# Optimization experiments

Hardware: AMD Instinct MI355X
Metric: run time of the kernel (lower is better)

The kernel has to match this reference:

```python
import jax, jax.numpy as jnp
import numpy as np

B, N, C, H = 2, 128, 256, 8
D = C // H
SCALE = D ** -0.5
LN_EPS = 1e-5


def _layernorm(x, g, b):
    mu = jnp.mean(x, axis=-1, keepdims=True)
    var = jnp.mean((x - mu) ** 2, axis=-1, keepdims=True)
    return (x - mu) * jax.lax.rsqrt(var + LN_EPS) * g + b


def setup_inputs() -> dict:
    key = jax.random.key(0)
    ks = jax.random.split(key, 12)
    s = 0.02
    return {
        "e": jax.random.normal(ks[0], (B, N, N, C), jnp.float32),
        "mask": jnp.zeros((B, N, N, H), jnp.float32),
        "ln_g": jnp.ones((C,), jnp.float32),
        "ln_b": jnp.zeros((C,), jnp.float32),
        "W_qkv_in": jax.random.normal(ks[1], (C, 3 * C), jnp.float32) * s,
        "b_qkv_in": jnp.zeros((3 * C,), jnp.float32),
        "W_E_in": jax.random.normal(ks[2], (C, H), jnp.float32) * s,
        "b_E_in": jnp.zeros((H,), jnp.float32),
        "W_qkv_out": jax.random.normal(ks[3], (C, 3 * C), jnp.float32) * s,
        "b_qkv_out": jnp.zeros((3 * C,), jnp.float32),
        "W_E_out": jax.random.normal(ks[4], (C, H), jnp.float32) * s,
        "b_E_out": jnp.zeros((H,), jnp.float32),
        "W_O": jax.random.normal(ks[5], (2 * C, C), jnp.float32) * s,
        "b_O": jnp.zeros((C,), jnp.float32),
    }


def reference(e, mask, ln_g, ln_b, W_qkv_in, b_qkv_in, W_E_in, b_E_in,
              W_qkv_out, b_qkv_out, W_E_out, b_E_out, W_O, b_O):
    b_, n, _, c = e.shape
    e_ln = _layernorm(e, ln_g, ln_b)

    def qkv(W, bias):
        z = e_ln @ W + bias  # [B,N,N,3C]
        q, k, v = jnp.split(z, 3, axis=-1)
        rs = lambda t: t.reshape(b_, n, n, D, H)
        return rs(q) * SCALE, rs(k), rs(v)

    # --- in pass ---
    Q, K, V = qkv(W_qkv_in, b_qkv_in)
    E_in = (e_ln @ W_E_in + b_E_in)[:, :, None, :, :]       # [B,N,1,N,H]
    H_in = jnp.einsum('bijdh,bjkdh->bijkh', Q, K) + E_in
    A_in = jax.nn.softmax(H_in + mask[:, :, None, :, :], axis=3)
    Va_in = jnp.einsum('bijkh,bjkdh->bijdh', A_in, V)

    # --- out pass ---
    Q, K, V = qkv(W_qkv_out, b_qkv_out)
    E_out = (e_ln @ W_E_out + b_E_out)[:, :, :, None, :]    # [B,N,N,1,H]
    H_out = jnp.einsum('bijdh,bkjdh->bkijh', Q, K) + E_out
    A_out = jax.nn.softmax(H_out + mask[:, :, :, None, :], axis=1)
    Va_out = jnp.einsum('bkijh,bkjdh->bijdh', A_out, V)

    Va = jnp.concatenate([Va_in, Va_out], axis=-1).reshape(b_, n, n, 2 * c)
    return Va @ W_O + b_O
```

## Files before the change

kernel.cpp:

```cpp
#include <hip/hip_runtime.h>

typedef unsigned short u16;
typedef __attribute__((ext_vector_type(8))) short bf16x8;
typedef __attribute__((ext_vector_type(4))) float f32x4;

#define SCALE 0.17677669529663687f

__device__ __forceinline__ float us2f(u16 u){ return __uint_as_float(((unsigned int)u)<<16); }
__device__ __forceinline__ u16 f2us(float f){
  unsigned int x = __float_as_uint(f);
  x += 0x7fffu + ((x>>16)&1u);
  return (u16)(x>>16);
}
__device__ __forceinline__ void gl_lds16(const u16* g, u16* l){
  __builtin_amdgcn_global_load_lds(
    (const __attribute__((address_space(1))) unsigned int*)g,
    (__attribute__((address_space(3))) unsigned int*)l, 16, 0, 0);
}

__global__ __launch_bounds__(256) void ln_kernel(const float* __restrict__ e, const float* __restrict__ g,
                                                 const float* __restrict__ bb, u16* __restrict__ eln){
  int t = threadIdx.x;
  int tok = blockIdx.x*4 + (t>>6);
  int lane = t & 63;
  int c0 = lane*4;
  float4 x = *(const float4*)(e + tok*256 + c0);
  float sum = x.x+x.y+x.z+x.w;
  float sq  = x.x*x.x + x.y*x.y + x.z*x.z + x.w*x.w;
  #pragma unroll
  for (int off=32; off>=1; off>>=1){ sum += __shfl_xor(sum, off); sq += __shfl_xor(sq, off); }
  float mu = sum * 0.00390625f;
  float var = sq * 0.00390625f - mu*mu;
  float rstd = rsqrtf(var + 1e-5f);
  float4 gv = *(const float4*)(g + c0);
  float4 bv = *(const float4*)(bb + c0);
  ushort4 o;
  o.x = f2us((x.x-mu)*rstd*gv.x + bv.x);
  o.y = f2us((x.y-mu)*rstd*gv.y + bv.y);
  o.z = f2us((x.z-mu)*rstd*gv.z + bv.z);
  o.w = f2us((x.w-mu)*rstd*gv.w + bv.w);
  *(ushort4*)(eln + tok*256 + c0) = o;
}

__global__ __launch_bounds__(256) void prep_all(const float* __restrict__ Wi, const float* __restrict__ WEi,
                                                const float* __restrict__ Wo, const float* __restrict__ WEo,
                                                const float* __restrict__ WO,
                                                u16* __restrict__ WtI, u16* __restrict__ WtO,
                                                u16* __restrict__ WOt){
  int idx = blockIdx.x*256 + threadIdx.x;
  if (idx < 425984){
    int which = idx >= 212992;
    int id2 = which ? idx - 212992 : idx;
    const float* W  = which ? Wo  : Wi;
    const float* WE = which ? WEo : WEi;
    u16* Wt = which ? WtO : WtI;
    int n = id2 >> 8, k = id2 & 255;
    float v;
    if (n < 768){
      int sec = n >> 8, r = n & 255, h = r >> 5, d = r & 31;
      v = W[k*768 + sec*256 + d*8 + h];
    } else if (n < 776) v = WE[k*8 + (n-768)];
    else v = 0.f;
    Wt[id2] = f2us(v);
  } else if (idx < 557056){
    int id2 = idx - 425984;
    int n = id2 >> 9, kp = id2 & 511;
    int pass = kp >> 8, h = (kp >> 5) & 7, d = kp & 31;
    int r = d*16 + pass*8 + h;
    WOt[id2] = f2us(WO[r*256 + n]);
  }
}

__global__ __launch_bounds__(256) void qkv_gemm(const u16* __restrict__ eln, const u16* __restrict__ Wt,
    const float* __restrict__ bqkv, const float* __restrict__ bE, const float* __restrict__ mask,
    u16* __restrict__ Qb, u16* __restrict__ Kb, u16* __restrict__ Vb, u16* __restrict__ biasP,
    int pass){
  __shared__ __align__(16) u16 smem[24576];
  int t = threadIdx.x;
  int g = blockIdx.x >> 8;
  int tmb = blockIdx.x & 255;
  int row0 = tmb*128, col0 = g*64;
  int w = t >> 6, lane = t & 63, quad = lane >> 4, l15 = lane & 15;
  int lr = lane >> 3, cc = lane & 7;
  int sw8 = (cc ^ lr) << 3;

  u16* A0 = smem;          u16* A1 = smem + 8192;
  u16* B0 = smem + 16384;  u16* B1 = smem + 20480;

  auto STAGE = [&](int kc, u16* Ab, u16* Bb){
    #pragma unroll
    for (int i=0; i<4; ++i){
      int lrow = w*32 + i*8;
      gl_lds16(eln + (row0 + lrow + lr)*256 + kc*64 + sw8, &Ab[lrow*64]);
    }
    #pragma unroll
    for (int j=0; j<2; ++j){
      int brow = w*16 + j*8;
      gl_lds16(Wt + (col0 + brow + lr)*256 + kc*64 + sw8, &Bb[brow*64]);
    }
  };

  f32x4 zero = {0.f,0.f,0.f,0.f};
  f32x4 acc[2][4];
  #pragma unroll
  for (int mt=0; mt<2; ++mt)
    #pragma unroll
    for (int nt=0; nt<4; ++nt) acc[mt][nt] = zero;

  STAGE(0, A0, B0);
  __syncthreads();

  #pragma unroll
  for (int kc=0; kc<4; ++kc){
    u16* Ac = (kc&1) ? A1 : A0;
    u16* Bc = (kc&1) ? B1 : B0;
    if (kc < 3) STAGE(kc+1, (kc&1)?A0:A1, (kc&1)?B0:B1);
    #pragma unroll
    for (int s=0; s<2; ++s){
      bf16x8 aF[2], bF[4];
      #pragma unroll
      for (int mt=0; mt<2; ++mt){
        int row = w*32 + mt*16 + l15;
        aF[mt] = *(const bf16x8*)&Ac[row*64 + ((((s<<2)+quad) ^ (l15&7))<<3)];
      }
      #pragma unroll
      for (int nt=0; nt<4; ++nt){
        int row = nt*16 + l15;
        bF[nt] = *(const bf16x8*)&Bc[row*64 + ((((s<<2)+quad) ^ (l15&7))<<3)];
      }
      #pragma unroll
      for (int mt=0; mt<2; ++mt)
        #pragma unroll
        for (int nt=0; nt<4; ++nt)
          acc[mt][nt] = __builtin_amdgcn_mfma_f32_16x16x32_bf16(aF[mt], bF[nt], acc[mt][nt], 0,0,0);
    }
    __syncthreads();
  }

  if (g < 12){
    int sec = g >> 2;
    float scl = (sec == 0) ? SCALE : 1.0f;
    u16* OutT = smem;
    #pragma unroll
    for (int mt=0; mt<2; ++mt){
      #pragma unroll
      for (int nt=0; nt<4; ++nt){
        int col = col0 + nt*16 + l15;
        int r = col & 255;
        float bias = bqkv[sec*256 + (r&31)*8 + (r>>5)];
        #pragma unroll
        for (int rr=0; rr<4; ++rr){
          int row = w*32 + mt*16 + quad*4 + rr;
          OutT[row*72 + nt*16 + l15] = f2us((acc[mt][nt][rr] + bias) * scl);
        }
      }
    }
    __syncthreads();
    u16* dst = (sec==0) ? Qb : (sec==1) ? Kb : Vb;
    int rbase = col0 & 255;
    int rrow = t >> 3, rc8 = (t & 7) * 8;
    #pragma unroll
    for (int k=0; k<4; ++k){
      int row = k*32 + rrow;
      uint4 v4 = *(const uint4*)&OutT[row*72 + rc8];
      *(uint4*)(dst + (row0 + row)*256 + rbase + rc8) = v4;
    }
  } else {
    if (l15 < 8){
      int h = l15;
      #pragma unroll
      for (int mt=0; mt<2; ++mt){
        #pragma unroll
        for (int rr=0; rr<4; ++rr){
          int tok = row0 + w*32 + mt*16 + quad*4 + rr;
          float v = acc[mt][0][rr];
          int bb = tok >> 14, t1 = (tok >> 7) & 127, t2 = tok & 127;
          int tq = pass ? t2 : t1, tk = pass ? t1 : t2;
          float bv2 = v + bE[h] + mask[tok*8 + h];
          biasP[(((bb*8 + h)*128 + tq)*128) + (tk & 15)*8 + (tk >> 4)] = f2us(bv2);
        }
      }
    }
  }
}

__global__ __launch_bounds__(256) void attn_mfma(const u16* __restrict__ Qb, const u16* __restrict__ Kb,
    const u16* __restrict__ Vb, const u16* __restrict__ biasP, u16* __restrict__ Va, int pass){
  __shared__ __align__(16) u16 uni[17408];
  __shared__ __align__(16) u16 VsT[32][136];
  typedef u16 row40[40];
  typedef u16 row136[136];
  row40*  Qs = (row40*)uni;
  row40*  Ks = (row40*)(uni + 5120);
  row136* Ps = (row136*)uni;
  int t = threadIdx.x;
  int bx = blockIdx.x;
  int h = bx & 7, j = (bx>>3) & 127, b = bx >> 10;

  #pragma unroll
  for (int it2=0; it2<2; ++it2){
    int idx = it2*256 + t;
    int row = idx >> 2, seg = idx & 3;
    int qoff  = ((b*128 + row)*128 + j)*256 + h*32 + seg*8;
    int kvtok = (pass == 0) ? ((b*128 + j)*128 + row) : ((b*128 + row)*128 + j);
    int kvoff = kvtok*256 + h*32 + seg*8;
    *(uint4*)&Qs[row][seg*8] = *(const uint4*)(Qb + qoff);
    *(uint4*)&Ks[row][seg*8] = *(const uint4*)(Kb + kvoff);
    uint4 vv = *(const uint4*)(Vb + kvoff);
    const u16* vp = (const u16*)&vv;
    int swc = (((row>>3) ^ seg) << 3) | (row & 7);
    #pragma unroll
    for (int q=0;q<8;++q) VsT[seg*8+q][swc] = vp[q];
  }
  __syncthreads();

  int w = t >> 6, lane = t & 63, quad = lane >> 4, l15 = lane & 15;
  bf16x8 aQ[2];
  #pragma unroll
  for (int it=0; it<2; ++it) aQ[it] = *(const bf16x8*)&Qs[w*32 + it*16 + l15][quad*8];
  f32x4 zero = {0.f,0.f,0.f,0.f};
  f32x4 S[2][8];
  #pragma unroll
  for (int tk=0; tk<8; ++tk){
    bf16x8 bK = *(const bf16x8*)&Ks[tk*16 + l15][quad*8];
    #pragma unroll
    for (int it=0; it<2; ++it)
      S[it][tk] = __builtin_amdgcn_mfma_f32_16x16x32_bf16(aQ[it], bK, zero, 0,0,0);
  }
  __syncthreads();
  const u16* bpP = biasP + ((b*8 + h)*128)*128;
  float inv[2][4];
  #pragma unroll
  for (int it=0; it<2; ++it){
    #pragma unroll
    for (int r=0; r<4; ++r){
      int i = w*32 + it*16 + quad*4 + r;
      uint4 b4 = *(const uint4*)(bpP + i*128 + l15*8);
      const u16* bu = (const u16*)&b4;
      float sv[8];
      #pragma unroll
      for (int tk=0; tk<8; ++tk) sv[tk] = S[it][tk][r] + us2f(bu[tk]);
      float m = sv[0];
      #pragma unroll
      for (int tk=1; tk<8; ++tk) m = fmaxf(m, sv[tk]);
      m = fmaxf(m, __shfl_xor(m,1)); m = fmaxf(m, __shfl_xor(m,2));
      m = fmaxf(m, __shfl_xor(m,4)); m = fmaxf(m, __shfl_xor(m,8));
      float l = 0.f;
      #pragma unroll
      for (int tk=0; tk<8; ++tk){ float p = __expf(sv[tk]-m); sv[tk] = p; l += p; }
      l += __shfl_xor(l,1); l += __shfl_xor(l,2); l += __shfl_xor(l,4); l += __shfl_xor(l,8);
      inv[it][r] = 1.0f / l;
      #pragma unroll
      for (int tk=0; tk<8; ++tk) Ps[i][tk*16 + l15] = f2us(sv[tk]);
    }
  }
  f32x4 O[2][2];
  #pragma unroll
  for (int it=0; it<2; ++it)
    #pragma unroll
    for (int dt=0; dt<2; ++dt) O[it][dt] = zero;
  #pragma unroll
  for (int kc=0; kc<4; ++kc){
    bf16x8 bV[2];
    #pragma unroll
    for (int dt=0; dt<2; ++dt){
      int key = (dt*2 + (l15>>3)) & 3;
      bV[dt] = *(const bf16x8*)&VsT[dt*16 + l15][((kc*4 + quad) ^ key) << 3];
    }
    #pragma unroll
    for (int it=0; it<2; ++it){
      bf16x8 aP = *(const bf16x8*)&Ps[w*32 + it*16 + l15][kc*32 + quad*8];
      #pragma unroll
      for (int dt=0; dt<2; ++dt)
        O[it][dt] = __builtin_amdgcn_mfma_f32_16x16x32_bf16(aP, bV[dt], O[it][dt], 0,0,0);
    }
  }
  #pragma unroll
  for (int it=0; it<2; ++it){
    #pragma unroll
    for (int r=0; r<4; ++r){
      int i = w*32 + it*16 + quad*4 + r;
      int obase = ((b*128 + i)*128 + j)*512 + pass*256 + h*32;
      #pragma unroll
      for (int dt=0; dt<2; ++dt)
        Va[obase + dt*16 + l15] = f2us(O[it][dt][r] * inv[it][r]);
    }
  }
}

__global__ __launch_bounds__(256) void out_gemm(const u16* __restrict__ Va, const u16* __restrict__ WOt,
                                                const float* __restrict__ bO, float* __restrict__ out){
  __shared__ __align__(16) u16 smem[24576];
  int t = threadIdx.x;
  int g = blockIdx.x >> 8;
  int tmb = blockIdx.x & 255;
  int row0 = tmb*128, col0 = g*64;
  int w = t >> 6, lane = t & 63, quad = lane >> 4, l15 = lane & 15;
  int lr = lane >> 3, cc = lane & 7;
  int sw8 = (cc ^ lr) << 3;

  u16* A0 = smem;          u16* A1 = smem + 8192;
  u16* B0 = smem + 16384;  u16* B1 = smem + 20480;

  auto STAGE = [&](int kc, u16* Ab, u16* Bb){
    #pragma unroll
    for (int i=0; i<4; ++i){
      int lrow = w*32 + i*8;
      gl_lds16(Va + (row0 + lrow + lr)*512 + kc*64 + sw8, &Ab[lrow*64]);
    }
    #pragma unroll
    for (int j=0; j<2; ++j){
      int brow = w*16 + j*8;
      gl_lds16(WOt + (col0 + brow + lr)*512 + kc*64 + sw8, &Bb[brow*64]);
    }
  };

  f32x4 zero = {0.f,0.f,0.f,0.f};
  f32x4 acc[2][4];
  #pragma unroll
  for (int mt=0; mt<2; ++mt)
    #pragma unroll
    for (int nt=0; nt<4; ++nt) acc[mt][nt] = zero;

  STAGE(0, A0, B0);
  __syncthreads();

  #pragma unroll
  for (int kc=0; kc<8; ++kc){
    u16* Ac = (kc&1) ? A1 : A0;
    u16* Bc = (kc&1) ? B1 : B0;
    if (kc < 7) STAGE(kc+1, (kc&1)?A0:A1, (kc&1)?B0:B1);
    #pragma unroll
    for (int s=0; s<2; ++s){
      bf16x8 aF[2], bF[4];
      #pragma unroll
      for (int mt=0; mt<2; ++mt){
        int row = w*32 + mt*16 + l15;
        aF[mt] = *(const bf16x8*)&Ac[row*64 + ((((s<<2)+quad) ^ (l15&7))<<3)];
      }
      #pragma unroll
      for (int nt=0; nt<4; ++nt){
        int row = nt*16 + l15;
        bF[nt] = *(const bf16x8*)&Bc[row*64 + ((((s<<2)+quad) ^ (l15&7))<<3)];
      }
      #pragma unroll
      for (int mt=0; mt<2; ++mt)
        #pragma unroll
        for (int nt=0; nt<4; ++nt)
          acc[mt][nt] = __builtin_amdgcn_mfma_f32_16x16x32_bf16(aF[mt], bF[nt], acc[mt][nt], 0,0,0);
    }
    __syncthreads();
  }
  #pragma unroll
  for (int mt=0; mt<2; ++mt){
    #pragma unroll
    for (int nt=0; nt<4; ++nt){
      int col = col0 + nt*16 + l15;
      float bias = bO[col];
      #pragma unroll
      for (int rr=0; rr<4; ++rr){
        int tok = row0 + w*32 + mt*16 + quad*4 + rr;
        out[tok*256 + col] = acc[mt][nt][rr] + bias;
      }
    }
  }
}

#define OFF_ELN   0u
#define OFF_QB    16777216u
#define OFF_KB    33554432u
#define OFF_VB    50331648u
#define OFF_VA    67108864u
#define OFF_BIASP 100663296u
#define OFF_WTI   101187584u
#define OFF_WTO   101613568u
#define OFF_WOT   102039552u

extern "C" void kernel_launch(void* const* d_in, const int* in_sizes, int n_in,
                              void* d_out, int out_size, void* d_ws, size_t ws_size,
                              hipStream_t stream) {
  (void)in_sizes; (void)n_in; (void)out_size; (void)ws_size;
  const float* e        = (const float*)d_in[0];
  const float* mask     = (const float*)d_in[1];
  const float* ln_g     = (const float*)d_in[2];
  const float* ln_b     = (const float*)d_in[3];
  const float* W_qkv_in = (const float*)d_in[4];
  const float* b_qkv_in = (const float*)d_in[5];
  const float* W_E_in   = (const float*)d_in[6];
  const float* b_E_in   = (const float*)d_in[7];
  const float* W_qkv_out= (const float*)d_in[8];
  const float* b_qkv_out= (const float*)d_in[9];
  const float* W_E_out  = (const float*)d_in[10];
  const float* b_E_out  = (const float*)d_in[11];
  const float* W_O      = (const float*)d_in[12];
  const float* b_O      = (const float*)d_in[13];

  char* ws = (char*)d_ws;
  u16*   eln   = (u16*)(ws + OFF_ELN);
  u16*   Qb    = (u16*)(ws + OFF_QB);
  u16*   Kb    = (u16*)(ws + OFF_KB);
  u16*   Vb    = (u16*)(ws + OFF_VB);
  u16*   Va    = (u16*)(ws + OFF_VA);
  u16*   biasP = (u16*)(ws + OFF_BIASP);
  u16*   WtI   = (u16*)(ws + OFF_WTI);
  u16*   WtO   = (u16*)(ws + OFF_WTO);
  u16*   WOt   = (u16*)(ws + OFF_WOT);

  float* out = (float*)d_out;

  hipLaunchKernelGGL(prep_all, dim3(2176), dim3(256), 0, stream,
                     W_qkv_in, W_E_in, W_qkv_out, W_E_out, W_O, WtI, WtO, WOt);
  hipLaunchKernelGGL(ln_kernel, dim3(8192), dim3(256), 0, stream, e, ln_g, ln_b, eln);

  hipLaunchKernelGGL(qkv_gemm, dim3(3328), dim3(256), 0, stream, eln, WtI, b_qkv_in, b_E_in, mask,
                     Qb, Kb, Vb, biasP, 0);
  hipLaunchKernelGGL(attn_mfma, dim3(2048), dim3(256), 0, stream, Qb, Kb, Vb, biasP, Va, 0);

  hipLaunchKernelGGL(qkv_gemm, dim3(3328), dim3(256), 0, stream, eln, WtO, b_qkv_out, b_E_out, mask,
                     Qb, Kb, Vb, biasP, 1);
  hipLaunchKernelGGL(attn_mfma, dim3(2048), dim3(256), 0, stream, Qb, Kb, Vb, biasP, Va, 1);

  hipLaunchKernelGGL(out_gemm, dim3(1024), dim3(256), 0, stream, Va, WOt, b_O, out);
}
```

Before: 250.8 us.

## Transpose Q/K/V layout at GEMM store, drop softmax max, fuse LN and prep

```diff
diff --git a/kernel.cpp b/kernel.cpp
--- a/kernel.cpp
+++ b/kernel.cpp
@@ -18,56 +18,58 @@
     (__attribute__((address_space(3))) unsigned int*)l, 16, 0, 0);
 }
 
-__global__ __launch_bounds__(256) void ln_kernel(const float* __restrict__ e, const float* __restrict__ g,
-                                                 const float* __restrict__ bb, u16* __restrict__ eln){
+__global__ __launch_bounds__(256) void ln_prep(const float* __restrict__ e, const float* __restrict__ g,
+                                               const float* __restrict__ bb, u16* __restrict__ eln,
+                                               const float* __restrict__ Wi, const float* __restrict__ WEi,
+                                               const float* __restrict__ Wo, const float* __restrict__ WEo,
+                                               const float* __restrict__ WO,
+                                               u16* __restrict__ WtI, u16* __restrict__ WtO,
+                                               u16* __restrict__ WOt){
+  int bid = blockIdx.x;
   int t = threadIdx.x;
-  int tok = blockIdx.x*4 + (t>>6);
-  int lane = t & 63;
-  int c0 = lane*4;
-  float4 x = *(const float4*)(e + tok*256 + c0);
-  float sum = x.x+x.y+x.z+x.w;
-  float sq  = x.x*x.x + x.y*x.y + x.z*x.z + x.w*x.w;
-  #pragma unroll
-  for (int off=32; off>=1; off>>=1){ sum += __shfl_xor(sum, off); sq += __shfl_xor(sq, off); }
-  float mu = sum * 0.00390625f;
-  float var = sq * 0.00390625f - mu*mu;
-  float rstd = rsqrtf(var + 1e-5f);
-  float4 gv = *(const float4*)(g + c0);
-  float4 bv = *(const float4*)(bb + c0);
-  ushort4 o;
-  o.x = f2us((x.x-mu)*rstd*gv.x + bv.x);
-  o.y = f2us((x.y-mu)*rstd*gv.y + bv.y);
-  o.z = f2us((x.z-mu)*rstd*gv.z + bv.z);
-  o.w = f2us((x.w-mu)*rstd*gv.w + bv.w);
-  *(ushort4*)(eln + tok*256 + c0) = o;
-}
-
-__global__ __launch_bounds__(256) void prep_all(const float* __restrict__ Wi, const float* __restrict__ WEi,
-                                                const float* __restrict__ Wo, const float* __restrict__ WEo,
-                                                const float* __restrict__ WO,
-                                                u16* __restrict__ WtI, u16* __restrict__ WtO,
-                                                u16* __restrict__ WOt){
-  int idx = blockIdx.x*256 + threadIdx.x;
-  if (idx < 425984){
-    int which = idx >= 212992;
-    int id2 = which ? idx - 212992 : idx;
-    const float* W  = which ? Wo  : Wi;
-    const float* WE = which ? WEo : WEi;
-    u16* Wt = which ? WtO : WtI;
-    int n = id2 >> 8, k = id2 & 255;
-    float v;
-    if (n < 768){
-      int sec = n >> 8, r = n & 255, h = r >> 5, d = r & 31;
-      v = W[k*768 + sec*256 + d*8 + h];
-    } else if (n < 776) v = WE[k*8 + (n-768)];
-    else v = 0.f;
-    Wt[id2] = f2us(v);
-  } else if (idx < 557056){
-    int id2 = idx - 425984;
-    int n = id2 >> 9, kp = id2 & 511;
-    int pass = kp >> 8, h = (kp >> 5) & 7, d = kp & 31;
-    int r = d*16 + pass*8 + h;
-    WOt[id2] = f2us(WO[r*256 + n]);
+  if (bid < 8192){
+    int tok = bid*4 + (t>>6);
+    int lane = t & 63;
+    int c0 = lane*4;
+    float4 x = *(const float4*)(e + tok*256 + c0);
+    float sum = x.x+x.y+x.z+x.w;
+    float sq  = x.x*x.x + x.y*x.y + x.z*x.z + x.w*x.w;
+    #pragma unroll
+    for (int off=32; off>=1; off>>=1){ sum += __shfl_xor(sum, off); sq += __shfl_xor(sq, off); }
+    float mu = sum * 0.00390625f;
+    float var = sq * 0.00390625f - mu*mu;
+    float rstd = rsqrtf(var + 1e-5f);
+    float4 gv = *(const float4*)(g + c0);
+    float4 bv = *(const float4*)(bb + c0);
+    ushort4 o;
+    o.x = f2us((x.x-mu)*rstd*gv.x + bv.x);
+    o.y = f2us((x.y-mu)*rstd*gv.y + bv.y);
+    o.z = f2us((x.z-mu)*rstd*gv.z + bv.z);
+    o.w = f2us((x.w-mu)*rstd*gv.w + bv.w);
+    *(ushort4*)(eln + tok*256 + c0) = o;
+  } else {
+    int idx = (bid - 8192)*256 + t;
+    if (idx < 425984){
+      int which = idx >= 212992;
+      int id2 = which ? idx - 212992 : idx;
+      const float* W  = which ? Wo  : Wi;
+      const float* WE = which ? WEo : WEi;
+      u16* Wt = which ? WtO : WtI;
+      int n = id2 >> 8, k = id2 & 255;
+      float v;
+      if (n < 768){
+        int sec = n >> 8, r = n & 255, h = r >> 5, d = r & 31;
+        v = W[k*768 + sec*256 + d*8 + h];
+      } else if (n < 776) v = WE[k*8 + (n-768)];
+      else v = 0.f;
+      Wt[id2] = f2us(v);
+    } else if (idx < 557056){
+      int id2 = idx - 425984;
+      int n = id2 >> 9, kp = id2 & 511;
+      int pass = kp >> 8, h = (kp >> 5) & 7, d = kp & 31;
+      int r = d*16 + pass*8 + h;
+      WOt[id2] = f2us(WO[r*256 + n]);
+    }
   }
 }
 
@@ -157,13 +159,16 @@
     }
     __syncthreads();
     u16* dst = (sec==0) ? Qb : (sec==1) ? Kb : Vb;
+    int tr = (sec==0) || pass;
+    int bq = tmb >> 7, iq = tmb & 127;
     int rbase = col0 & 255;
     int rrow = t >> 3, rc8 = (t & 7) * 8;
     #pragma unroll
     for (int k=0; k<4; ++k){
       int row = k*32 + rrow;
       uint4 v4 = *(const uint4*)&OutT[row*72 + rc8];
-      *(uint4*)(dst + (row0 + row)*256 + rbase + rc8) = v4;
+      int tok = tr ? (bq*16384 + row*128 + iq) : (row0 + row);
+      *(uint4*)(dst + tok*256 + rbase + rc8) = v4;
     }
   } else {
     if (l15 < 8){
@@ -197,16 +202,15 @@
   int bx = blockIdx.x;
   int h = bx & 7, j = (bx>>3) & 127, b = bx >> 10;
 
+  int base = ((b*128 + j)*128)*256 + h*32;
   #pragma unroll
   for (int it2=0; it2<2; ++it2){
     int idx = it2*256 + t;
     int row = idx >> 2, seg = idx & 3;
-    int qoff  = ((b*128 + row)*128 + j)*256 + h*32 + seg*8;
-    int kvtok = (pass == 0) ? ((b*128 + j)*128 + row) : ((b*128 + row)*128 + j);
-    int kvoff = kvtok*256 + h*32 + seg*8;
-    *(uint4*)&Qs[row][seg*8] = *(const uint4*)(Qb + qoff);
-    *(uint4*)&Ks[row][seg*8] = *(const uint4*)(Kb + kvoff);
-    uint4 vv = *(const uint4*)(Vb + kvoff);
+    int off = base + row*256 + seg*8;
+    *(uint4*)&Qs[row][seg*8] = *(const uint4*)(Qb + off);
+    *(uint4*)&Ks[row][seg*8] = *(const uint4*)(Kb + off);
+    uint4 vv = *(const uint4*)(Vb + off);
     const u16* vp = (const u16*)&vv;
     int swc = (((row>>3) ^ seg) << 3) | (row & 7);
     #pragma unroll
@@ -237,17 +241,13 @@
       int i = w*32 + it*16 + quad*4 + r;
       uint4 b4 = *(const uint4*)(bpP + i*128 + l15*8);
       const u16* bu = (const u16*)&b4;
+      float l = 0.f;
       float sv[8];
       #pragma unroll
-      for (int tk=0; tk<8; ++tk) sv[tk] = S[it][tk][r] + us2f(bu[tk]);
-      float m = sv[0];
-      #pragma unroll
-      for (int tk=1; tk<8; ++tk) m = fmaxf(m, sv[tk]);
-      m = fmaxf(m, __shfl_xor(m,1)); m = fmaxf(m, __shfl_xor(m,2));
-      m = fmaxf(m, __shfl_xor(m,4)); m = fmaxf(m, __shfl_xor(m,8));
-      float l = 0.f;
-      #pragma unroll
-      for (int tk=0; tk<8; ++tk){ float p = __expf(sv[tk]-m); sv[tk] = p; l += p; }
+      for (int tk=0; tk<8; ++tk){
+        float p = __expf(S[it][tk][r] + us2f(bu[tk]));
+        sv[tk] = p; l += p;
+      }
       l += __shfl_xor(l,1); l += __shfl_xor(l,2); l += __shfl_xor(l,4); l += __shfl_xor(l,8);
       inv[it][r] = 1.0f / l;
       #pragma unroll
@@ -408,9 +408,9 @@
 
   float* out = (float*)d_out;
 
-  hipLaunchKernelGGL(prep_all, dim3(2176), dim3(256), 0, stream,
+  hipLaunchKernelGGL(ln_prep, dim3(10368), dim3(256), 0, stream,
+                     e, ln_g, ln_b, eln,
                      W_qkv_in, W_E_in, W_qkv_out, W_E_out, W_O, WtI, WtO, WOt);
-  hipLaunchKernelGGL(ln_kernel, dim3(8192), dim3(256), 0, stream, e, ln_g, ln_b, eln);
 
   hipLaunchKernelGGL(qkv_gemm, dim3(3328), dim3(256), 0, stream, eln, WtI, b_qkv_in, b_E_in, mask,
                      Qb, Kb, Vb, biasP, 0);
```

New measurement: 243.8 us. 2.8% less time.
